# Performance work log

Measured on AMD Instinct MI355X. Metric: run time of the kernel, lower is better.

Reference implementation:

```python
import jax, jax.numpy as jnp
import numpy as np

BS, TGT, SRC = 16, 100, 100
M, N, H = 512, 512, 256  # query_size, key_size, hidden (min//2)


def setup_inputs() -> dict:
    key = jax.random.key(0)
    ks = jax.random.split(key, 7)
    s1 = 1.0 / np.sqrt(M + N)  # torch Linear init scale for layer 1 (fan_in = 1024)
    s2 = 1.0 / np.sqrt(H)
    return {
        "query": jax.random.normal(ks[0], (BS, TGT, M), jnp.float32),
        "keys": jax.random.normal(ks[1], (BS, SRC, N), jnp.float32),
        # W1 (H, M+N) split into key-part and query-part (concat order is (keys, query))
        "Wk": jax.random.uniform(ks[2], (N, H), jnp.float32, -s1, s1),
        "Wq": jax.random.uniform(ks[3], (M, H), jnp.float32, -s1, s1),
        "b1": jax.random.uniform(ks[4], (H,), jnp.float32, -s1, s1),
        "W2": jax.random.uniform(ks[5], (H, 1), jnp.float32, -s2, s2),
        "b2": jax.random.uniform(ks[6], (1,), jnp.float32, -s2, s2),
    }


def reference(query, keys, Wk, Wq, b1, W2, b2):
    # Equivalent to concat([keys_bcast, query_bcast], -1) @ W1 + b1:
    # apply the split weight to each side, then broadcast-add over the grid.
    hk = jnp.einsum("bsn,nh->bsh", keys, Wk)   # (bs, src, H)
    hq = jnp.einsum("btm,mh->bth", query, Wq)  # (bs, tgt, H)
    h = jnp.tanh(hk[:, :, None, :] + hq[:, None, :, :] + b1)  # (bs, src, tgt, H)
    score = jnp.tanh(jnp.einsum("bsth,ho->bsto", h, W2) + b2)  # (bs, src, tgt, 1)
    return score.squeeze(-1)  # (bs, src, tgt)
```

## Files before the change

kernel.cpp:

```cpp
#include <hip/hip_runtime.h>

#define TGT 100
#define SRC 100
#define KDIM 512
#define HH 256
#define ROWS 1600
#define LOG2E2 2.8853900817779268f

typedef __attribute__((ext_vector_type(8))) short bf16x8;
typedef __attribute__((ext_vector_type(4))) float f32x4;

#define EQT_OFF 409600
#define PK_FLOAT_OFF 819200
#define APK_SHORTS 1638400

static __device__ __forceinline__ short f2b(float f) {
    union { float f; unsigned u; } v; v.f = f;
    return (short)((v.u + 0x7FFFu + ((v.u >> 16) & 1u)) >> 16);
}

__global__ __launch_bounds__(256) void prep_kernel(
    const float* __restrict__ query, const float* __restrict__ keys,
    const float* __restrict__ Wk, const float* __restrict__ Wq,
    short* __restrict__ Apk, short* __restrict__ Bpk)
{
    const int tid = blockIdx.x * 256 + threadIdx.x;
    if (tid < 204800) {
        const int lane = tid & 63;
        const int rest = tid >> 6;
        const int kk = rest & 15;
        const int rg = rest >> 4;
        const float* A = (rg >= 100) ? query : keys;
        const int r = (rg % 100) * 16 + (lane & 15);
        const int kb = kk * 32 + (lane >> 4) * 8;
        const float* src = A + (size_t)r * KDIM + kb;
        f32x4 a0 = *(const f32x4*)src;
        f32x4 a1 = *(const f32x4*)(src + 4);
        bf16x8 v;
        #pragma unroll
        for (int j = 0; j < 4; ++j) { v[j] = f2b(a0[j]); v[j + 4] = f2b(a1[j]); }
        *(bf16x8*)(Apk + (size_t)tid * 8) = v;
    } else if (tid < 237568) {
        const int t2 = tid - 204800;
        const int lane = t2 & 63;
        const int rest = t2 >> 6;
        const int kk = rest & 15;
        const int ht = (rest >> 4) & 15;
        const float* W = (rest >> 8) ? Wq : Wk;
        const int kb = kk * 32 + (lane >> 4) * 8;
        const int col = ht * 16 + (lane & 15);
        const float* wp = W + (size_t)kb * HH + col;
        bf16x8 v;
        #pragma unroll
        for (int j = 0; j < 8; ++j) v[j] = f2b(wp[(size_t)j * HH]);
        *(bf16x8*)(Bpk + (size_t)t2 * 8) = v;
    }
}

__global__ __launch_bounds__(256) void gemm_exp_kernel(
    const short* __restrict__ Apk, const short* __restrict__ Bpk,
    const float* __restrict__ b1,
    float* __restrict__ Ek, float* __restrict__ EqT)
{
    const int lane = threadIdx.x & 63;
    const int w = blockIdx.x * 4 + (threadIdx.x >> 6);
    const int rt = w >> 4;
    const int ht = w & 15;
    const int isq = rt >= 100;
    const short* ap = Apk + ((size_t)(rt * 16) * 64 + lane) * 8;
    const short* bp = Bpk + ((size_t)((isq * 16 + ht) * 16) * 64 + lane) * 8;

    f32x4 acc = {0.f, 0.f, 0.f, 0.f};
    #pragma unroll
    for (int kk = 0; kk < 16; ++kk) {
        bf16x8 af = *(const bf16x8*)(ap + (size_t)kk * 512);
        bf16x8 bf = *(const bf16x8*)(bp + (size_t)kk * 512);
        acc = __builtin_amdgcn_mfma_f32_16x16x32_bf16(af, bf, acc, 0, 0, 0);
    }

    const int m = lane & 15, q = lane >> 4;
    const int hc = ht * 16 + m;
    const int r0 = (isq ? rt - 100 : rt) * 16;
    if (!isq) {
        #pragma unroll
        for (int r = 0; r < 4; ++r) {
            const int row = r0 + q * 4 + r;
            Ek[(size_t)row * HH + hc] = __builtin_amdgcn_exp2f(LOG2E2 * acc[r]);
        }
    } else {
        const float bb = b1[hc];
        #pragma unroll
        for (int r = 0; r < 4; ++r) {
            const int row = r0 + q * 4 + r;
            EqT[(size_t)hc * ROWS + row] =
                __builtin_amdgcn_exp2f(LOG2E2 * (acc[r] + bb));
        }
    }
}

__global__ __launch_bounds__(256) void score_kernel(
    const float* __restrict__ Ek, const float* __restrict__ EqT,
    const float* __restrict__ W2, const float* __restrict__ B2,
    float* __restrict__ out)
{
    __shared__ float red[4][4][64];
    const int lane = threadIdx.x & 63;
    const int wv = threadIdx.x >> 6;
    const int bx = blockIdx.x;
    const int tc = (bx & 1) << 6;
    const int g  = bx >> 1;
    const int sq = g % 25;
    const int b  = g / 25;
    const int s0 = sq * 4;
    const int t  = tc + lane;
    const int tcl = t < TGT ? t : TGT - 1;
    const int h0 = wv * 64;

    const float* __restrict__ ek = Ek + (size_t)(b * SRC + s0) * HH + h0;
    const float* __restrict__ eq = EqT + (size_t)h0 * ROWS + (size_t)b * TGT + tcl;
    const float* __restrict__ w2 = W2 + h0;

    float acc0 = 0.f, acc1 = 0.f, acc2 = 0.f, acc3 = 0.f;
    #pragma unroll 4
    for (int hp = 0; hp < 32; ++hp) {
        const int h = hp * 2;
        const float2 w  = *(const float2*)(w2 + h);
        const float  e0 = eq[(size_t)h * ROWS];
        const float  e1 = eq[(size_t)(h + 1) * ROWS];
        const float2 k0 = *(const float2*)(ek + h);
        const float2 k1 = *(const float2*)(ek + HH + h);
        const float2 k2 = *(const float2*)(ek + 2 * HH + h);
        const float2 k3 = *(const float2*)(ek + 3 * HH + h);
        acc0 = fmaf(w.x, __builtin_amdgcn_rcpf(fmaf(k0.x, e0, 1.f)), acc0);
        acc1 = fmaf(w.x, __builtin_amdgcn_rcpf(fmaf(k1.x, e0, 1.f)), acc1);
        acc2 = fmaf(w.x, __builtin_amdgcn_rcpf(fmaf(k2.x, e0, 1.f)), acc2);
        acc3 = fmaf(w.x, __builtin_amdgcn_rcpf(fmaf(k3.x, e0, 1.f)), acc3);
        acc0 = fmaf(w.y, __builtin_amdgcn_rcpf(fmaf(k0.y, e1, 1.f)), acc0);
        acc1 = fmaf(w.y, __builtin_amdgcn_rcpf(fmaf(k1.y, e1, 1.f)), acc1);
        acc2 = fmaf(w.y, __builtin_amdgcn_rcpf(fmaf(k2.y, e1, 1.f)), acc2);
        acc3 = fmaf(w.y, __builtin_amdgcn_rcpf(fmaf(k3.y, e1, 1.f)), acc3);
    }
    red[0][wv][lane] = acc0;
    red[1][wv][lane] = acc1;
    red[2][wv][lane] = acc2;
    red[3][wv][lane] = acc3;
    __syncthreads();

    float a = red[wv][0][lane] + red[wv][1][lane] + red[wv][2][lane] + red[wv][3][lane];
    float sw = W2[lane] + W2[lane + 64] + W2[lane + 128] + W2[lane + 192];
    #pragma unroll
    for (int off = 32; off; off >>= 1) sw += __shfl_xor(sw, off, 64);
    const float x = sw - 2.f * a + B2[0];
    const float gx = __builtin_amdgcn_exp2f(LOG2E2 * x);
    if (t < TGT)
        out[((size_t)b * SRC + s0 + wv) * TGT + t] =
            1.f - 2.f * __builtin_amdgcn_rcpf(gx + 1.f);
}

extern "C" void kernel_launch(void* const* d_in, const int* in_sizes, int n_in,
                              void* d_out, int out_size, void* d_ws, size_t ws_size,
                              hipStream_t stream) {
    const float* query = (const float*)d_in[0];
    const float* keys  = (const float*)d_in[1];
    const float* Wk    = (const float*)d_in[2];
    const float* Wq    = (const float*)d_in[3];
    const float* b1    = (const float*)d_in[4];
    const float* W2    = (const float*)d_in[5];
    const float* B2    = (const float*)d_in[6];
    float* out = (float*)d_out;

    float* Ek  = (float*)d_ws;
    float* EqT = Ek + EQT_OFF;
    short* Apk = (short*)(Ek + PK_FLOAT_OFF);
    short* Bpk = Apk + APK_SHORTS;

    prep_kernel<<<928, 256, 0, stream>>>(query, keys, Wk, Wq, Apk, Bpk);
    gemm_exp_kernel<<<800, 256, 0, stream>>>(Apk, Bpk, b1, Ek, EqT);
    score_kernel<<<800, 256, 0, stream>>>(Ek, EqT, W2, B2, out);
}
```

Baseline: 93.29 us.

## Fuse bf16 packing into GEMM kernel with shared-memory weight tile

Removes the separate prep kernel and converts inputs to bf16 on the fly inside the GEMM kernel. Each block stages its 16-column weight tile into shared memory as packed bf16, and each wave converts its fp32 activation rows in registers before issuing MFMA. This drops one launch and the round trip of packed bf16 buffers through global memory. In exchange, every block re-reads and re-converts its strided weight tile, which duplicates work across the 50 row-group blocks that share it.

Measured after the change: 99.07 us. +6.2%, slower.

```diff
diff --git a/kernel.cpp b/kernel.cpp
--- a/kernel.cpp
+++ b/kernel.cpp
@@ -11,76 +11,64 @@
 typedef __attribute__((ext_vector_type(4))) float f32x4;
 
 #define EQT_OFF 409600
-#define PK_FLOAT_OFF 819200
-#define APK_SHORTS 1638400
 
 static __device__ __forceinline__ short f2b(float f) {
     union { float f; unsigned u; } v; v.f = f;
     return (short)((v.u + 0x7FFFu + ((v.u >> 16) & 1u)) >> 16);
 }
 
-__global__ __launch_bounds__(256) void prep_kernel(
+__global__ __launch_bounds__(256) void gemm_exp_fused(
     const float* __restrict__ query, const float* __restrict__ keys,
     const float* __restrict__ Wk, const float* __restrict__ Wq,
-    short* __restrict__ Apk, short* __restrict__ Bpk)
+    const float* __restrict__ b1,
+    float* __restrict__ Ek, float* __restrict__ EqT)
 {
-    const int tid = blockIdx.x * 256 + threadIdx.x;
-    if (tid < 204800) {
-        const int lane = tid & 63;
-        const int rest = tid >> 6;
-        const int kk = rest & 15;
-        const int rg = rest >> 4;
-        const float* A = (rg >= 100) ? query : keys;
-        const int r = (rg % 100) * 16 + (lane & 15);
-        const int kb = kk * 32 + (lane >> 4) * 8;
-        const float* src = A + (size_t)r * KDIM + kb;
-        f32x4 a0 = *(const f32x4*)src;
-        f32x4 a1 = *(const f32x4*)(src + 4);
-        bf16x8 v;
-        #pragma unroll
-        for (int j = 0; j < 4; ++j) { v[j] = f2b(a0[j]); v[j + 4] = f2b(a1[j]); }
-        *(bf16x8*)(Apk + (size_t)tid * 8) = v;
-    } else if (tid < 237568) {
-        const int t2 = tid - 204800;
-        const int lane = t2 & 63;
-        const int rest = t2 >> 6;
-        const int kk = rest & 15;
-        const int ht = (rest >> 4) & 15;
-        const float* W = (rest >> 8) ? Wq : Wk;
-        const int kb = kk * 32 + (lane >> 4) * 8;
-        const int col = ht * 16 + (lane & 15);
-        const float* wp = W + (size_t)kb * HH + col;
+    __shared__ short Bf[8192];
+    const int tid  = threadIdx.x;
+    const int lane = tid & 63;
+    const int wv   = tid >> 6;
+    const int bx   = blockIdx.x;
+    const int rtg  = bx >> 4;
+    const int ht   = bx & 15;
+    const int isq  = rtg >= 25;
+    const float* __restrict__ W = isq ? Wq : Wk;
+
+    #pragma unroll
+    for (int i = 0; i < 4; ++i) {
+        const int f  = tid + 256 * i;
+        const int kk = f >> 6;
+        const int ln = f & 63;
+        const float* wp = W + (size_t)(kk * 32 + (ln >> 4) * 8) * HH
+                            + ht * 16 + (ln & 15);
         bf16x8 v;
         #pragma unroll
         for (int j = 0; j < 8; ++j) v[j] = f2b(wp[(size_t)j * HH]);
-        *(bf16x8*)(Bpk + (size_t)t2 * 8) = v;
+        *(bf16x8*)(Bf + (size_t)f * 8) = v;
     }
-}
+    __syncthreads();
 
-__global__ __launch_bounds__(256) void gemm_exp_kernel(
-    const short* __restrict__ Apk, const short* __restrict__ Bpk,
-    const float* __restrict__ b1,
-    float* __restrict__ Ek, float* __restrict__ EqT)
-{
-    const int lane = threadIdx.x & 63;
-    const int w = blockIdx.x * 4 + (threadIdx.x >> 6);
-    const int rt = w >> 4;
-    const int ht = w & 15;
-    const int isq = rt >= 100;
-    const short* ap = Apk + ((size_t)(rt * 16) * 64 + lane) * 8;
-    const short* bp = Bpk + ((size_t)((isq * 16 + ht) * 16) * 64 + lane) * 8;
+    const int rt = rtg * 4 + wv;
+    const int rl = isq ? rt - 100 : rt;
+    const float* __restrict__ A = isq ? query : keys;
+    const float* arow = A + (size_t)(rl * 16 + (lane & 15)) * KDIM
+                          + (lane >> 4) * 8;
+    const short* bfp = Bf + lane * 8;
 
     f32x4 acc = {0.f, 0.f, 0.f, 0.f};
     #pragma unroll
     for (int kk = 0; kk < 16; ++kk) {
-        bf16x8 af = *(const bf16x8*)(ap + (size_t)kk * 512);
-        bf16x8 bf = *(const bf16x8*)(bp + (size_t)kk * 512);
-        acc = __builtin_amdgcn_mfma_f32_16x16x32_bf16(af, bf, acc, 0, 0, 0);
+        f32x4 a0 = *(const f32x4*)(arow + kk * 32);
+        f32x4 a1 = *(const f32x4*)(arow + kk * 32 + 4);
+        bf16x8 af;
+        #pragma unroll
+        for (int j = 0; j < 4; ++j) { af[j] = f2b(a0[j]); af[j + 4] = f2b(a1[j]); }
+        bf16x8 bfr = *(const bf16x8*)(bfp + (size_t)kk * 512);
+        acc = __builtin_amdgcn_mfma_f32_16x16x32_bf16(af, bfr, acc, 0, 0, 0);
     }
 
     const int m = lane & 15, q = lane >> 4;
     const int hc = ht * 16 + m;
-    const int r0 = (isq ? rt - 100 : rt) * 16;
+    const int r0 = rl * 16;
     if (!isq) {
         #pragma unroll
         for (int r = 0; r < 4; ++r) {
@@ -171,10 +159,7 @@
 
     float* Ek  = (float*)d_ws;
     float* EqT = Ek + EQT_OFF;
-    short* Apk = (short*)(Ek + PK_FLOAT_OFF);
-    short* Bpk = Apk + APK_SHORTS;
 
-    prep_kernel<<<928, 256, 0, stream>>>(query, keys, Wk, Wq, Apk, Bpk);
-    gemm_exp_kernel<<<800, 256, 0, stream>>>(Apk, Bpk, b1, Ek, EqT);
+    gemm_exp_fused<<<800, 256, 0, stream>>>(query, keys, Wk, Wq, b1, Ek, EqT);
     score_kernel<<<800, 256, 0, stream>>>(Ek, EqT, W2, B2, out);
 }
```
